# Optimization experiments

Measured on AMD Instinct MI355X. Metric: run time of the kernel, lower is better.

## Reference

```python
import jax, jax.numpy as jnp
import numpy as np

N = 100000   # nodes
D = 128      # in_feats
H = 128      # hidden_size
E = 500000   # message edges
EP = 100000  # positive pair edges
EN = 500000  # negative pair edges


def setup_inputs() -> dict:
    key = jax.random.key(0)
    ks = jax.random.split(key, 20)
    s = 1.0 / np.sqrt(H)
    f32 = jnp.float32
    inp = {
        "x": jax.random.normal(ks[0], (N, D), f32),
        "src": jax.random.randint(ks[1], (E,), 0, N, jnp.int32),
        "dst": jax.random.randint(ks[2], (E,), 0, N, jnp.int32),
        "pos_src": jax.random.randint(ks[3], (EP,), 0, N, jnp.int32),
        "pos_dst": jax.random.randint(ks[4], (EP,), 0, N, jnp.int32),
        "neg_src": jax.random.randint(ks[5], (EN,), 0, N, jnp.int32),
        "neg_dst": jax.random.randint(ks[6], (EN,), 0, N, jnp.int32),
        # SAGEConv layer 0 (in->hid) and layer 1 (hid->hid)
        "W_self0": jax.random.normal(ks[7], (D, H), f32) * s,
        "W_neigh0": jax.random.normal(ks[8], (D, H), f32) * s,
        "b0": jnp.zeros((H,), f32),
        "W_self1": jax.random.normal(ks[9], (H, H), f32) * s,
        "W_neigh1": jax.random.normal(ks[10], (H, H), f32) * s,
        "b1": jnp.zeros((H,), f32),
        # EdgeDecoder MLP: hid->hid->hid->1
        "dW1": jax.random.normal(ks[11], (H, H), f32) * s,
        "db1": jnp.zeros((H,), f32),
        "dW2": jax.random.normal(ks[12], (H, H), f32) * s,
        "db2": jnp.zeros((H,), f32),
        "dW3": jax.random.normal(ks[13], (H, 1), f32) * s,
        "db3": jnp.zeros((1,), f32),
    }
    return inp


def _sage_mean(h, src, dst, W_self, W_neigh, b, n_nodes):
    # mean-aggregate neighbor features: gather src feats, segment-sum over dst
    agg = jax.ops.segment_sum(h[src], dst, num_segments=n_nodes)       # [N, d]
    deg = jax.ops.segment_sum(jnp.ones((src.shape[0],), h.dtype), dst,
                              num_segments=n_nodes)                     # [N]
    h_neigh = agg / jnp.maximum(deg, 1.0)[:, None]
    return h @ W_self + h_neigh @ W_neigh + b


def _edge_decode(h, e_src, e_dst, W1, b1, W2, b2, W3, b3):
    z = h[e_src] * h[e_dst]                    # [E_pair, H]
    z = jax.nn.relu(z @ W1 + b1)
    z = jax.nn.relu(z @ W2 + b2)
    return z @ W3 + b3                         # [E_pair, 1]


def reference(x, src, dst, pos_src, pos_dst, neg_src, neg_dst,
              W_self0, W_neigh0, b0, W_self1, W_neigh1, b1,
              dW1, db1, dW2, db2, dW3, db3):
    n = x.shape[0]
    h = jax.nn.relu(_sage_mean(x, src, dst, W_self0, W_neigh0, b0, n))
    h = _sage_mean(h, src, dst, W_self1, W_neigh1, b1, n)  # no act on last layer
    h_pos = _edge_decode(h, pos_src, pos_dst, dW1, db1, dW2, db2, dW3, db3)
    h_neg = _edge_decode(h, neg_src, neg_dst, dW1, db1, dW2, db2, dW3, db3)
    return (h_pos, h_neg)
```

## Files before the change

### kernel.cpp

```cpp
#include <hip/hip_runtime.h>
#include <hip/hip_bf16.h>

#define HD 128

typedef unsigned int u32;
typedef unsigned short u16;
typedef __attribute__((ext_vector_type(8))) short short8;
typedef __attribute__((ext_vector_type(4))) float f32x4;

__device__ __forceinline__ float bf2f(u16 u) {
    return __uint_as_float(((u32)u) << 16);
}
__device__ __forceinline__ u16 f2bf(float f) {
    u32 u = __float_as_uint(f);
    u32 r = (u + 0x7fffu + ((u >> 16) & 1u)) >> 16;
    return (u16)r;
}
__device__ __forceinline__ u32 pk2bf(float lo, float hi) {
    __hip_bfloat162 h = __float22bfloat162_rn(make_float2(lo, hi));
    union { __hip_bfloat162 h; u32 u; } cv; cv.h = h;
    return cv.u;
}
__device__ __forceinline__ u32 hmul2(u32 a, u32 b) {
    union { u32 u; __hip_bfloat162 h; } x, y, r;
    x.u = a; y.u = b;
    r.h = __hmul2(x.h, y.h);
    return r.u;
}
__device__ __forceinline__ float ldf(const void* p, size_t i, bool f32m) {
    return f32m ? ((const float*)p)[i] : bf2f(((const u16*)p)[i]);
}
__device__ __forceinline__ int swz(int row, int col) {
    return row * 128 + ((((col >> 3) ^ (row & 7)) << 3) | (col & 7));
}
__device__ __forceinline__ void acc8_bf16(uint4 v, float* a) {
    a[0] += __uint_as_float(v.x << 16); a[1] += __uint_as_float(v.x & 0xffff0000u);
    a[2] += __uint_as_float(v.y << 16); a[3] += __uint_as_float(v.y & 0xffff0000u);
    a[4] += __uint_as_float(v.z << 16); a[5] += __uint_as_float(v.z & 0xffff0000u);
    a[6] += __uint_as_float(v.w << 16); a[7] += __uint_as_float(v.w & 0xffff0000u);
}

__global__ void detect_mode(const u32* __restrict__ x, int* __restrict__ mode) {
    __shared__ int cnt_s;
    if (threadIdx.x == 0) cnt_s = 0;
    __syncthreads();
    u32 e = (x[threadIdx.x] >> 23) & 0xFFu;
    if (e >= 90u && e < 170u) atomicAdd(&cnt_s, 1);
    __syncthreads();
    if (threadIdx.x == 0) mode[0] = (cnt_s >= 128) ? 1 : 0;
}

__global__ void pack_w6(const void* __restrict__ W0, const void* __restrict__ W1,
                        const void* __restrict__ W2, const void* __restrict__ W3,
                        const void* __restrict__ W4, const void* __restrict__ W5,
                        u16* __restrict__ out, const int* __restrict__ gmode) {
    const bool f32m = gmode[0] != 0;
    int gid = blockIdx.x * 256 + threadIdx.x;
    if (gid >= 6 * 16384) return;
    int sel = gid >> 14, idx = gid & 16383;
    const void* W = sel == 0 ? W0 : sel == 1 ? W1 : sel == 2 ? W2 :
                    sel == 3 ? W3 : sel == 4 ? W4 : W5;
    int j = idx & 7, lane = (idx >> 3) & 63, ks = (idx >> 9) & 3, nt = idx >> 11;
    int k = ks * 32 + (lane >> 4) * 8 + j;
    int n = nt * 16 + (lane & 15);
    out[gid] = f2bf(ldf(W, (size_t)k * HD + n, f32m));
}

__global__ void cnt_count(const int* __restrict__ dst, int* __restrict__ cnt, int e) {
    int i = blockIdx.x * 256 + threadIdx.x;
    if (i < e) atomicAdd(&cnt[dst[i]], 1);
}

__global__ void scan_blocks(const int* __restrict__ cnt, int* __restrict__ rowptr,
                            int* __restrict__ bsum, int n) {
    __shared__ int s[256];
    int t = threadIdx.x, gid = blockIdx.x * 256 + t;
    int v = (gid < n) ? cnt[gid] : 0;
    s[t] = v; __syncthreads();
    #pragma unroll
    for (int off = 1; off < 256; off <<= 1) {
        int x = (t >= off) ? s[t - off] : 0;
        __syncthreads();
        s[t] += x;
        __syncthreads();
    }
    if (gid < n) rowptr[gid] = s[t] - v;
    if (t == 255) bsum[blockIdx.x] = s[255];
}

__global__ void scan_bsum(int* __restrict__ bsum, int nb) {
    __shared__ int s[1024];
    __shared__ int carry;
    int t = threadIdx.x;
    if (t == 0) carry = 0;
    __syncthreads();
    for (int base = 0; base < nb; base += 1024) {
        int i = base + t;
        int v = (i < nb) ? bsum[i] : 0;
        s[t] = v; __syncthreads();
        #pragma unroll
        for (int off = 1; off < 1024; off <<= 1) {
            int x = (t >= off) ? s[t - off] : 0;
            __syncthreads();
            s[t] += x;
            __syncthreads();
        }
        if (i < nb) bsum[i] = carry + s[t] - v;
        __syncthreads();
        if (t == 0) carry += s[1023];
        __syncthreads();
    }
}

__global__ void scan_add(int* __restrict__ rowptr, const int* __restrict__ bsum,
                         int* __restrict__ cur, int n, int e) {
    int gid = blockIdx.x * 256 + threadIdx.x;
    if (gid < n) {
        int v = rowptr[gid] + bsum[blockIdx.x];
        rowptr[gid] = v;
        cur[gid] = v;
    } else if (gid == n) {
        rowptr[n] = e;
    }
}

__global__ void csr_fill(const int* __restrict__ src, const int* __restrict__ dst,
                         int* __restrict__ cur, int* __restrict__ cidx, int e) {
    int i = blockIdx.x * 256 + threadIdx.x;
    if (i >= e) return;
    int p = atomicAdd(&cur[dst[i]], 1);
    cidx[p] = src[i];
}

template <bool RELU>
__global__ __launch_bounds__(256) void sage_mfma(
    const void* __restrict__ X, const int* __restrict__ rowptr,
    const int* __restrict__ cidx,
    const u16* __restrict__ Wsp, const u16* __restrict__ Wnp,
    const void* __restrict__ bias, u16* __restrict__ hout,
    const int* __restrict__ gmode, int use_mode, int n) {
    __shared__ u16 z[64 * 128];
    const bool f32m = gmode[0] != 0;
    const bool inf32 = use_mode && f32m;
    const int t = threadIdx.x;
    const int n0 = blockIdx.x * 64;
    const int lane = t & 63;
    const int w = t >> 6;
    const int cl = lane & 15, quad = lane >> 4;
    const int l16 = lane & 15, g = lane >> 4;

    #pragma unroll
    for (int i = 0; i < 4; i++) {
        int idx = t + i * 256;
        int e = idx >> 4, sg = (idx & 15) * 8;
        int node = n0 + e;
        uint4 p = make_uint4(0, 0, 0, 0);
        if (node < n) {
            if (inf32) {
                const float* xp = (const float*)X + (size_t)node * HD + sg;
                float4 v0 = *(const float4*)xp, v1 = *(const float4*)(xp + 4);
                p.x = pk2bf(v0.x, v0.y); p.y = pk2bf(v0.z, v0.w);
                p.z = pk2bf(v1.x, v1.y); p.w = pk2bf(v1.z, v1.w);
            } else {
                p = *(const uint4*)((const u16*)X + (size_t)node * HD + sg);
            }
        }
        *(uint4*)&z[swz(e, sg)] = p;
    }
    __syncthreads();

    f32x4 acc[2][4];
    #pragma unroll
    for (int ft = 0; ft < 2; ft++) {
        int f0 = w * 32 + ft * 16 + quad * 4;
        f32x4 bv;
        bv[0] = ldf(bias, f0 + 0, f32m);
        bv[1] = ldf(bias, f0 + 1, f32m);
        bv[2] = ldf(bias, f0 + 2, f32m);
        bv[3] = ldf(bias, f0 + 3, f32m);
        #pragma unroll
        for (int et = 0; et < 4; et++) acc[ft][et] = bv;
    }
    #pragma unroll
    for (int ks = 0; ks < 4; ks++) {
        short8 a[2], b[4];
        #pragma unroll
        for (int ft = 0; ft < 2; ft++)
            a[ft] = ((const short8*)Wsp)[((w * 2 + ft) * 4 + ks) * 64 + lane];
        #pragma unroll
        for (int et = 0; et < 4; et++)
            b[et] = *(const short8*)&z[swz(et * 16 + cl, ks * 32 + quad * 8)];
        #pragma unroll
        for (int ft = 0; ft < 2; ft++)
            #pragma unroll
            for (int et = 0; et < 4; et++)
                acc[ft][et] = __builtin_amdgcn_mfma_f32_16x16x32_bf16(
                    a[ft], b[et], acc[ft][et], 0, 0, 0);
    }
    __syncthreads();

    #pragma unroll 1
    for (int r = 0; r < 4; r++) {
        int e = w * 16 + r * 4 + g;
        int node = n0 + e;
        float a[8] = {0.f, 0.f, 0.f, 0.f, 0.f, 0.f, 0.f, 0.f};
        int deg = 0;
        if (node < n) {
            int s0 = rowptr[node], s1 = rowptr[node + 1];
            deg = s1 - s0;
            int i = s0;
            if (inf32) {
                for (; i + 1 < s1; i += 2) {
                    const float* pA = (const float*)X + (size_t)cidx[i] * HD + l16 * 8;
                    const float* pB = (const float*)X + (size_t)cidx[i + 1] * HD + l16 * 8;
                    float4 a0 = *(const float4*)pA, a1 = *(const float4*)(pA + 4);
                    float4 b0 = *(const float4*)pB, b1 = *(const float4*)(pB + 4);
                    a[0] += a0.x + b0.x; a[1] += a0.y + b0.y;
                    a[2] += a0.z + b0.z; a[3] += a0.w + b0.w;
                    a[4] += a1.x + b1.x; a[5] += a1.y + b1.y;
                    a[6] += a1.z + b1.z; a[7] += a1.w + b1.w;
                }
                if (i < s1) {
                    const float* pA = (const float*)X + (size_t)cidx[i] * HD + l16 * 8;
                    float4 a0 = *(const float4*)pA, a1 = *(const float4*)(pA + 4);
                    a[0] += a0.x; a[1] += a0.y; a[2] += a0.z; a[3] += a0.w;
                    a[4] += a1.x; a[5] += a1.y; a[6] += a1.z; a[7] += a1.w;
                }
            } else {
                for (; i + 1 < s1; i += 2) {
                    uint4 vA = *(const uint4*)((const u16*)X + (size_t)cidx[i] * HD + l16 * 8);
                    uint4 vB = *(const uint4*)((const u16*)X + (size_t)cidx[i + 1] * HD + l16 * 8);
                    acc8_bf16(vA, a);
                    acc8_bf16(vB, a);
                }
                if (i < s1) {
                    uint4 vA = *(const uint4*)((const u16*)X + (size_t)cidx[i] * HD + l16 * 8);
                    acc8_bf16(vA, a);
                }
            }
        }
        float iv = 1.f / fmaxf((float)deg, 1.f);
        uint4 o;
        o.x = pk2bf(a[0] * iv, a[1] * iv);
        o.y = pk2bf(a[2] * iv, a[3] * iv);
        o.z = pk2bf(a[4] * iv, a[5] * iv);
        o.w = pk2bf(a[6] * iv, a[7] * iv);
        *(uint4*)&z[swz(e, l16 * 8)] = o;
    }
    __syncthreads();

    #pragma unroll
    for (int ks = 0; ks < 4; ks++) {
        short8 a[2], b[4];
        #pragma unroll
        for (int ft = 0; ft < 2; ft++)
            a[ft] = ((const short8*)Wnp)[((w * 2 + ft) * 4 + ks) * 64 + lane];
        #pragma unroll
        for (int et = 0; et < 4; et++)
            b[et] = *(const short8*)&z[swz(et * 16 + cl, ks * 32 + quad * 8)];
        #pragma unroll
        for (int ft = 0; ft < 2; ft++)
            #pragma unroll
            for (int et = 0; et < 4; et++)
                acc[ft][et] = __builtin_amdgcn_mfma_f32_16x16x32_bf16(
                    a[ft], b[et], acc[ft][et], 0, 0, 0);
    }
    __syncthreads();

    #pragma unroll
    for (int ft = 0; ft < 2; ft++) {
        int f0 = w * 32 + ft * 16 + quad * 4;
        #pragma unroll
        for (int et = 0; et < 4; et++) {
            f32x4 v = acc[ft][et];
            float v0 = RELU ? fmaxf(v[0], 0.f) : v[0];
            float v1 = RELU ? fmaxf(v[1], 0.f) : v[1];
            float v2 = RELU ? fmaxf(v[2], 0.f) : v[2];
            float v3 = RELU ? fmaxf(v[3], 0.f) : v[3];
            *(uint2*)&z[swz(et * 16 + cl, f0)] =
                make_uint2(pk2bf(v0, v1), pk2bf(v2, v3));
        }
    }
    __syncthreads();
    #pragma unroll
    for (int i = 0; i < 4; i++) {
        int idx = t + i * 256;
        int e = idx >> 4, sg = (idx & 15) * 8;
        int node = n0 + e;
        if (node < n)
            *(uint4*)&hout[(size_t)node * HD + sg] = *(const uint4*)&z[swz(e, sg)];
    }
}

__global__ __launch_bounds__(256) void edge_decode_mfma(
    const u16* __restrict__ h,
    const int* __restrict__ psrc, const int* __restrict__ pdst, int ep, int PB,
    const int* __restrict__ nsrc, const int* __restrict__ ndst, int en,
    const u16* __restrict__ W1p, const void* __restrict__ b1,
    const u16* __restrict__ W2p, const void* __restrict__ b2,
    const void* __restrict__ W3, const void* __restrict__ b3,
    void* __restrict__ out, const int* __restrict__ gmode) {
    __shared__ u16 zA[64 * 128];
    __shared__ float psum[256];
    const bool f32m = gmode[0] != 0;
    const int t = threadIdx.x;
    const int b = blockIdx.x;
    const int* esrc; const int* edst; int e0, obase, ne;
    if (b < PB) { esrc = psrc; edst = pdst; e0 = b * 64;        obase = 0;  ne = ep; }
    else        { esrc = nsrc; edst = ndst; e0 = (b - PB) * 64; obase = ep; ne = en; }
    const int lane = t & 63;
    const int w = t >> 6;
    const int cl = lane & 15, quad = lane >> 4;

    #pragma unroll
    for (int i = 0; i < 4; i++) {
        int idx = t + i * 256;
        int e = idx >> 4, sg = (idx & 15) * 8;
        int eg = e0 + e;
        uint4 z = make_uint4(0, 0, 0, 0);
        if (eg < ne) {
            int s = esrc[eg], d = edst[eg];
            uint4 a  = *(const uint4*)(h + (size_t)s * HD + sg);
            uint4 bv = *(const uint4*)(h + (size_t)d * HD + sg);
            z.x = hmul2(a.x, bv.x); z.y = hmul2(a.y, bv.y);
            z.z = hmul2(a.z, bv.z); z.w = hmul2(a.w, bv.w);
        }
        *(uint4*)&zA[swz(e, sg)] = z;
    }
    __syncthreads();

    f32x4 acc[2][4];
    #pragma unroll
    for (int ft = 0; ft < 2; ft++) {
        int f0 = w * 32 + ft * 16 + quad * 4;
        f32x4 bv;
        bv[0] = ldf(b1, f0 + 0, f32m);
        bv[1] = ldf(b1, f0 + 1, f32m);
        bv[2] = ldf(b1, f0 + 2, f32m);
        bv[3] = ldf(b1, f0 + 3, f32m);
        #pragma unroll
        for (int et = 0; et < 4; et++) acc[ft][et] = bv;
    }
    #pragma unroll
    for (int ks = 0; ks < 4; ks++) {
        short8 a[2], bb[4];
        #pragma unroll
        for (int ft = 0; ft < 2; ft++)
            a[ft] = ((const short8*)W1p)[((w * 2 + ft) * 4 + ks) * 64 + lane];
        #pragma unroll
        for (int et = 0; et < 4; et++)
            bb[et] = *(const short8*)&zA[swz(et * 16 + cl, ks * 32 + quad * 8)];
        #pragma unroll
        for (int ft = 0; ft < 2; ft++)
            #pragma unroll
            for (int et = 0; et < 4; et++)
                acc[ft][et] = __builtin_amdgcn_mfma_f32_16x16x32_bf16(
                    a[ft], bb[et], acc[ft][et], 0, 0, 0);
    }
    __syncthreads();

    #pragma unroll
    for (int ft = 0; ft < 2; ft++) {
        int f0 = w * 32 + ft * 16 + quad * 4;
        #pragma unroll
        for (int et = 0; et < 4; et++) {
            f32x4 v = acc[ft][et];
            *(uint2*)&zA[swz(et * 16 + cl, f0)] = make_uint2(
                pk2bf(fmaxf(v[0], 0.f), fmaxf(v[1], 0.f)),
                pk2bf(fmaxf(v[2], 0.f), fmaxf(v[3], 0.f)));
        }
    }
    __syncthreads();

    #pragma unroll
    for (int ft = 0; ft < 2; ft++) {
        int f0 = w * 32 + ft * 16 + quad * 4;
        f32x4 bv;
        bv[0] = ldf(b2, f0 + 0, f32m);
        bv[1] = ldf(b2, f0 + 1, f32m);
        bv[2] = ldf(b2, f0 + 2, f32m);
        bv[3] = ldf(b2, f0 + 3, f32m);
        #pragma unroll
        for (int et = 0; et < 4; et++) acc[ft][et] = bv;
    }
    #pragma unroll
    for (int ks = 0; ks < 4; ks++) {
        short8 a[2], bb[4];
        #pragma unroll
        for (int ft = 0; ft < 2; ft++)
            a[ft] = ((const short8*)W2p)[((w * 2 + ft) * 4 + ks) * 64 + lane];
        #pragma unroll
        for (int et = 0; et < 4; et++)
            bb[et] = *(const short8*)&zA[swz(et * 16 + cl, ks * 32 + quad * 8)];
        #pragma unroll
        for (int ft = 0; ft < 2; ft++)
            #pragma unroll
            for (int et = 0; et < 4; et++)
                acc[ft][et] = __builtin_amdgcn_mfma_f32_16x16x32_bf16(
                    a[ft], bb[et], acc[ft][et], 0, 0, 0);
    }
    float p[4] = {0.f, 0.f, 0.f, 0.f};
    #pragma unroll
    for (int ft = 0; ft < 2; ft++) {
        int f0 = w * 32 + ft * 16 + quad * 4;
        float w3v0 = ldf(W3, f0 + 0, f32m);
        float w3v1 = ldf(W3, f0 + 1, f32m);
        float w3v2 = ldf(W3, f0 + 2, f32m);
        float w3v3 = ldf(W3, f0 + 3, f32m);
        #pragma unroll
        for (int et = 0; et < 4; et++) {
            f32x4 v = acc[ft][et];
            p[et] = fmaf(fmaxf(v[0], 0.f), w3v0, p[et]);
            p[et] = fmaf(fmaxf(v[1], 0.f), w3v1, p[et]);
            p[et] = fmaf(fmaxf(v[2], 0.f), w3v2, p[et]);
            p[et] = fmaf(fmaxf(v[3], 0.f), w3v3, p[et]);
        }
    }
    #pragma unroll
    for (int et = 0; et < 4; et++) {
        p[et] += __shfl_xor(p[et], 16);
        p[et] += __shfl_xor(p[et], 32);
    }
    if (lane < 16) {
        #pragma unroll
        for (int et = 0; et < 4; et++)
            psum[w * 64 + et * 16 + lane] = p[et];
    }
    __syncthreads();
    if (t < 64) {
        int eg = e0 + t;
        if (eg < ne) {
            float sum = ldf(b3, 0, f32m) + (psum[t] + psum[64 + t])
                      + (psum[128 + t] + psum[192 + t]);
            if (f32m) ((float*)out)[obase + eg] = sum;
            else      ((u16*)out)[obase + eg]   = f2bf(sum);
        }
    }
}

extern "C" void kernel_launch(void* const* d_in, const int* in_sizes, int n_in,
                              void* d_out, int out_size, void* d_ws, size_t ws_size,
                              hipStream_t stream) {
    const void* x      = d_in[0];
    const int* src     = (const int*)d_in[1];
    const int* dst     = (const int*)d_in[2];
    const int* pos_src = (const int*)d_in[3];
    const int* pos_dst = (const int*)d_in[4];
    const int* neg_src = (const int*)d_in[5];
    const int* neg_dst = (const int*)d_in[6];
    const void* Ws0 = d_in[7];
    const void* Wn0 = d_in[8];
    const void* b0  = d_in[9];
    const void* Ws1 = d_in[10];
    const void* Wn1 = d_in[11];
    const void* b1  = d_in[12];
    const void* dW1 = d_in[13];
    const void* db1 = d_in[14];
    const void* dW2 = d_in[15];
    const void* db2 = d_in[16];
    const void* dW3 = d_in[17];
    const void* db3 = d_in[18];

    const int n  = in_sizes[0] / HD;
    const int e  = in_sizes[1];
    const int ep = in_sizes[3];
    const int en = in_sizes[5];
    const int NB = (n + 255) / 256;
    const int PB = (ep + 63) / 64, NDB = (en + 63) / 64;

    char* base = (char*)d_ws;
    u16* h2 = (u16*)d_ws;
    u16* h1 = h2 + (size_t)n * HD;
    size_t off = (size_t)n * HD * 4;
    int* mode = (int*)(base + off);      off += 16;
    int* rowptr = (int*)(base + off);    off += (size_t)(n + 1) * 4; off = (off + 15) & ~(size_t)15;
    int* cur = (int*)(base + off);       off += (size_t)n * 4;       off = (off + 15) & ~(size_t)15;
    int* cidx = (int*)(base + off);      off += (size_t)e * 4;       off = (off + 15) & ~(size_t)15;
    int* bsum = (int*)(base + off);      off += (size_t)NB * 4;      off = (off + 15) & ~(size_t)15;
    u16* Wpk  = (u16*)(base + off);
    u16* W1p  = Wpk;
    u16* W2p  = Wpk + 16384;
    u16* Ws0p = Wpk + 2 * 16384;
    u16* Wn0p = Wpk + 3 * 16384;
    u16* Ws1p = Wpk + 4 * 16384;
    u16* Wn1p = Wpk + 5 * 16384;

    detect_mode<<<dim3(1), dim3(256), 0, stream>>>((const u32*)x, mode);

    hipMemsetAsync(cur, 0, (size_t)n * 4, stream);
    cnt_count<<<dim3((e + 255) / 256), dim3(256), 0, stream>>>(dst, cur, e);
    scan_blocks<<<dim3(NB), dim3(256), 0, stream>>>(cur, rowptr, bsum, n);
    scan_bsum<<<dim3(1), dim3(1024), 0, stream>>>(bsum, NB);
    scan_add<<<dim3((n + 256) / 256), dim3(256), 0, stream>>>(rowptr, bsum, cur, n, e);
    csr_fill<<<dim3((e + 255) / 256), dim3(256), 0, stream>>>(src, dst, cur, cidx, e);

    pack_w6<<<dim3(384), dim3(256), 0, stream>>>(dW1, dW2, Ws0, Wn0, Ws1, Wn1, Wpk, mode);

    sage_mfma<true><<<dim3((n + 63) / 64), dim3(256), 0, stream>>>(
        x, rowptr, cidx, Ws0p, Wn0p, b0, h1, mode, 1, n);

    sage_mfma<false><<<dim3((n + 63) / 64), dim3(256), 0, stream>>>(
        h1, rowptr, cidx, Ws1p, Wn1p, b1, h2, mode, 0, n);

    edge_decode_mfma<<<dim3(PB + NDB), dim3(256), 0, stream>>>(
        h2, pos_src, pos_dst, ep, PB, neg_src, neg_dst, en,
        W1p, db1, W2p, db2, dW3, db3, d_out, mode);
}
```

Before: 349.6 us.

## Pre-cast input to bf16, stage CSR indices in LDS, interleave two-node gathers

Adds a cast_x kernel that converts the fp32 input features to bf16 once, so the first SAGE layer's neighbour gathers read half as many bytes as the fp32 rows they read before. Inside sage_mfma, each block stages its rowptr slice and up to 896 column indices in shared memory, with a fallback to global memory past that cap. The aggregation loop now processes two destination nodes at once, giving more independent gather loads in flight. The cost is an extra full pass over x and workspace reuse of the h2 buffer as the bf16 copy of x.

```diff
diff --git a/kernel.cpp b/kernel.cpp
--- a/kernel.cpp
+++ b/kernel.cpp
@@ -2,6 +2,7 @@
 #include <hip/hip_bf16.h>
 
 #define HD 128
+#define CIDX_CAP 896
 
 typedef unsigned int u32;
 typedef unsigned short u16;
@@ -39,6 +40,14 @@
     a[4] += __uint_as_float(v.z << 16); a[5] += __uint_as_float(v.z & 0xffff0000u);
     a[6] += __uint_as_float(v.w << 16); a[7] += __uint_as_float(v.w & 0xffff0000u);
 }
+__device__ __forceinline__ uint4 ldrow16(const u16* __restrict__ Xb, int node, int colo) {
+    return *(const uint4*)(Xb + (size_t)node * HD + colo);
+}
+__device__ __forceinline__ int gc(const int* __restrict__ cidx,
+                                  const int* cx_s, int cbase, int j) {
+    int o = j - cbase;
+    return (o < CIDX_CAP) ? cx_s[o] : cidx[j];
+}
 
 __global__ void detect_mode(const u32* __restrict__ x, int* __restrict__ mode) {
     __shared__ int cnt_s;
@@ -48,6 +57,21 @@
     if (e >= 90u && e < 170u) atomicAdd(&cnt_s, 1);
     __syncthreads();
     if (threadIdx.x == 0) mode[0] = (cnt_s >= 128) ? 1 : 0;
+}
+
+__global__ void cast_x(const float* __restrict__ x, u16* __restrict__ xb,
+                       const int* __restrict__ gmode, int total8) {
+    if (gmode[0] == 0) return;
+    int i = blockIdx.x * 256 + threadIdx.x;
+    int stride = gridDim.x * 256;
+    for (; i < total8; i += stride) {
+        const float* p = x + (size_t)i * 8;
+        float4 v0 = *(const float4*)p, v1 = *(const float4*)(p + 4);
+        uint4 o;
+        o.x = pk2bf(v0.x, v0.y); o.y = pk2bf(v0.z, v0.w);
+        o.z = pk2bf(v1.x, v1.y); o.w = pk2bf(v1.z, v1.w);
+        *(uint4*)(xb + (size_t)i * 8) = o;
+    }
 }
 
 __global__ void pack_w6(const void* __restrict__ W0, const void* __restrict__ W1,
@@ -134,14 +158,16 @@
 
 template <bool RELU>
 __global__ __launch_bounds__(256) void sage_mfma(
-    const void* __restrict__ X, const int* __restrict__ rowptr,
-    const int* __restrict__ cidx,
+    const void* __restrict__ X, const u16* __restrict__ Xc,
+    const int* __restrict__ rowptr, const int* __restrict__ cidx,
     const u16* __restrict__ Wsp, const u16* __restrict__ Wnp,
     const void* __restrict__ bias, u16* __restrict__ hout,
-    const int* __restrict__ gmode, int use_mode, int n) {
+    const int* __restrict__ gmode, int n) {
     __shared__ u16 z[64 * 128];
+    __shared__ int rp_s[65];
+    __shared__ int cx_s[CIDX_CAP];
     const bool f32m = gmode[0] != 0;
-    const bool inf32 = use_mode && f32m;
+    const u16* Xb = f32m ? Xc : (const u16*)X;
     const int t = threadIdx.x;
     const int n0 = blockIdx.x * 64;
     const int lane = t & 63;
@@ -149,25 +175,29 @@
     const int cl = lane & 15, quad = lane >> 4;
     const int l16 = lane & 15, g = lane >> 4;
 
+    if (t < 65) {
+        int idx = n0 + t;
+        rp_s[t] = rowptr[idx < n ? idx : n];
+    }
+
     #pragma unroll
     for (int i = 0; i < 4; i++) {
         int idx = t + i * 256;
         int e = idx >> 4, sg = (idx & 15) * 8;
         int node = n0 + e;
         uint4 p = make_uint4(0, 0, 0, 0);
-        if (node < n) {
-            if (inf32) {
-                const float* xp = (const float*)X + (size_t)node * HD + sg;
-                float4 v0 = *(const float4*)xp, v1 = *(const float4*)(xp + 4);
-                p.x = pk2bf(v0.x, v0.y); p.y = pk2bf(v0.z, v0.w);
-                p.z = pk2bf(v1.x, v1.y); p.w = pk2bf(v1.z, v1.w);
-            } else {
-                p = *(const uint4*)((const u16*)X + (size_t)node * HD + sg);
-            }
-        }
+        if (node < n)
+            p = *(const uint4*)(Xb + (size_t)node * HD + sg);
         *(uint4*)&z[swz(e, sg)] = p;
     }
     __syncthreads();
+
+    const int cbase = rp_s[0];
+    {
+        int ccnt = rp_s[64] - cbase;
+        if (ccnt > CIDX_CAP) ccnt = CIDX_CAP;
+        for (int j = t; j < ccnt; j += 256) cx_s[j] = cidx[cbase + j];
+    }
 
     f32x4 acc[2][4];
     #pragma unroll
@@ -200,52 +230,65 @@
     __syncthreads();
 
     #pragma unroll 1
-    for (int r = 0; r < 4; r++) {
-        int e = w * 16 + r * 4 + g;
-        int node = n0 + e;
-        float a[8] = {0.f, 0.f, 0.f, 0.f, 0.f, 0.f, 0.f, 0.f};
-        int deg = 0;
-        if (node < n) {
-            int s0 = rowptr[node], s1 = rowptr[node + 1];
-            deg = s1 - s0;
-            int i = s0;
-            if (inf32) {
-                for (; i + 1 < s1; i += 2) {
-                    const float* pA = (const float*)X + (size_t)cidx[i] * HD + l16 * 8;
-                    const float* pB = (const float*)X + (size_t)cidx[i + 1] * HD + l16 * 8;
-                    float4 a0 = *(const float4*)pA, a1 = *(const float4*)(pA + 4);
-                    float4 b0 = *(const float4*)pB, b1 = *(const float4*)(pB + 4);
-                    a[0] += a0.x + b0.x; a[1] += a0.y + b0.y;
-                    a[2] += a0.z + b0.z; a[3] += a0.w + b0.w;
-                    a[4] += a1.x + b1.x; a[5] += a1.y + b1.y;
-                    a[6] += a1.z + b1.z; a[7] += a1.w + b1.w;
-                }
-                if (i < s1) {
-                    const float* pA = (const float*)X + (size_t)cidx[i] * HD + l16 * 8;
-                    float4 a0 = *(const float4*)pA, a1 = *(const float4*)(pA + 4);
-                    a[0] += a0.x; a[1] += a0.y; a[2] += a0.z; a[3] += a0.w;
-                    a[4] += a1.x; a[5] += a1.y; a[6] += a1.z; a[7] += a1.w;
-                }
-            } else {
-                for (; i + 1 < s1; i += 2) {
-                    uint4 vA = *(const uint4*)((const u16*)X + (size_t)cidx[i] * HD + l16 * 8);
-                    uint4 vB = *(const uint4*)((const u16*)X + (size_t)cidx[i + 1] * HD + l16 * 8);
-                    acc8_bf16(vA, a);
-                    acc8_bf16(vB, a);
-                }
-                if (i < s1) {
-                    uint4 vA = *(const uint4*)((const u16*)X + (size_t)cidx[i] * HD + l16 * 8);
-                    acc8_bf16(vA, a);
-                }
-            }
-        }
-        float iv = 1.f / fmaxf((float)deg, 1.f);
-        uint4 o;
-        o.x = pk2bf(a[0] * iv, a[1] * iv);
-        o.y = pk2bf(a[2] * iv, a[3] * iv);
-        o.z = pk2bf(a[4] * iv, a[5] * iv);
-        o.w = pk2bf(a[6] * iv, a[7] * iv);
-        *(uint4*)&z[swz(e, l16 * 8)] = o;
+    for (int r2 = 0; r2 < 2; r2++) {
+        int eA = w * 16 + r2 * 8 + g;
+        int eB = eA + 4;
+        int sA0 = rp_s[eA], sA1 = rp_s[eA + 1];
+        int sB0 = rp_s[eB], sB1 = rp_s[eB + 1];
+        float aA[8] = {0.f, 0.f, 0.f, 0.f, 0.f, 0.f, 0.f, 0.f};
+        float aB[8] = {0.f, 0.f, 0.f, 0.f, 0.f, 0.f, 0.f, 0.f};
+        int iA = sA0, iB = sB0;
+        const int colo = l16 * 8;
+        while (iA + 1 < sA1 && iB + 1 < sB1) {
+            int c0 = gc(cidx, cx_s, cbase, iA);
+            int c1 = gc(cidx, cx_s, cbase, iA + 1);
+            int c2 = gc(cidx, cx_s, cbase, iB);
+            int c3 = gc(cidx, cx_s, cbase, iB + 1);
+            uint4 v0 = ldrow16(Xb, c0, colo);
+            uint4 v1 = ldrow16(Xb, c1, colo);
+            uint4 v2 = ldrow16(Xb, c2, colo);
+            uint4 v3 = ldrow16(Xb, c3, colo);
+            acc8_bf16(v0, aA); acc8_bf16(v1, aA);
+            acc8_bf16(v2, aB); acc8_bf16(v3, aB);
+            iA += 2; iB += 2;
+        }
+        for (; iA + 1 < sA1; iA += 2) {
+            int c0 = gc(cidx, cx_s, cbase, iA);
+            int c1 = gc(cidx, cx_s, cbase, iA + 1);
+            uint4 v0 = ldrow16(Xb, c0, colo);
+            uint4 v1 = ldrow16(Xb, c1, colo);
+            acc8_bf16(v0, aA); acc8_bf16(v1, aA);
+        }
+        if (iA < sA1) {
+            int c0 = gc(cidx, cx_s, cbase, iA);
+            uint4 v0 = ldrow16(Xb, c0, colo);
+            acc8_bf16(v0, aA);
+        }
+        for (; iB + 1 < sB1; iB += 2) {
+            int c0 = gc(cidx, cx_s, cbase, iB);
+            int c1 = gc(cidx, cx_s, cbase, iB + 1);
+            uint4 v0 = ldrow16(Xb, c0, colo);
+            uint4 v1 = ldrow16(Xb, c1, colo);
+            acc8_bf16(v0, aB); acc8_bf16(v1, aB);
+        }
+        if (iB < sB1) {
+            int c0 = gc(cidx, cx_s, cbase, iB);
+            uint4 v0 = ldrow16(Xb, c0, colo);
+            acc8_bf16(v0, aB);
+        }
+        float ivA = 1.f / fmaxf((float)(sA1 - sA0), 1.f);
+        float ivB = 1.f / fmaxf((float)(sB1 - sB0), 1.f);
+        uint4 oA, oB;
+        oA.x = pk2bf(aA[0] * ivA, aA[1] * ivA);
+        oA.y = pk2bf(aA[2] * ivA, aA[3] * ivA);
+        oA.z = pk2bf(aA[4] * ivA, aA[5] * ivA);
+        oA.w = pk2bf(aA[6] * ivA, aA[7] * ivA);
+        oB.x = pk2bf(aB[0] * ivB, aB[1] * ivB);
+        oB.y = pk2bf(aB[2] * ivB, aB[3] * ivB);
+        oB.z = pk2bf(aB[4] * ivB, aB[5] * ivB);
+        oB.w = pk2bf(aB[6] * ivB, aB[7] * ivB);
+        *(uint4*)&z[swz(eA, colo)] = oA;
+        *(uint4*)&z[swz(eB, colo)] = oB;
     }
     __syncthreads();
 
@@ -471,6 +514,7 @@
     char* base = (char*)d_ws;
     u16* h2 = (u16*)d_ws;
     u16* h1 = h2 + (size_t)n * HD;
+    u16* xb = h2;
     size_t off = (size_t)n * HD * 4;
     int* mode = (int*)(base + off);      off += 16;
     int* rowptr = (int*)(base + off);    off += (size_t)(n + 1) * 4; off = (off + 15) & ~(size_t)15;
@@ -496,11 +540,14 @@
 
     pack_w6<<<dim3(384), dim3(256), 0, stream>>>(dW1, dW2, Ws0, Wn0, Ws1, Wn1, Wpk, mode);
 
+    cast_x<<<dim3(2048), dim3(256), 0, stream>>>(
+        (const float*)x, xb, mode, n * (HD / 8));
+
     sage_mfma<true><<<dim3((n + 63) / 64), dim3(256), 0, stream>>>(
-        x, rowptr, cidx, Ws0p, Wn0p, b0, h1, mode, 1, n);
+        x, xb, rowptr, cidx, Ws0p, Wn0p, b0, h1, mode, n);
 
     sage_mfma<false><<<dim3((n + 63) / 64), dim3(256), 0, stream>>>(
-        h1, rowptr, cidx, Ws1p, Wn1p, b1, h2, mode, 0, n);
+        h1, h1, rowptr, cidx, Ws1p, Wn1p, b1, h2, mode, n);
 
     edge_decode_mfma<<<dim3(PB + NDB), dim3(256), 0, stream>>>(
         h2, pos_src, pos_dst, ep, PB, neg_src, neg_dst, en,
```

Result: no change. 350.9 us (+0.4%).

## Split SAGE layers into separate gather-mean and GEMM kernels with bf16 input cast

Applied to the files above, without the earlier changes.

Moves the neighbor mean aggregation out of the fused SAGE MFMA kernel into a standalone agg_mean kernel with 16 rows per block and 4-way unrolled gathers. The layer-0 input is first cast to bf16 once, so gathers read half-size rows instead of fp32 ones. The GEMM kernel then reads both the self and mean tiles from global memory. This aims to raise occupancy and gather parallelism, decoupled from the MFMA tile, at the cost of extra kernel launches and an intermediate mean buffer written and read per layer. sage_gemm writes its output in place into its own input buffer; this looks safe because each block reads only its own 64 rows before overwriting them.

```diff
diff --git a/kernel.cpp b/kernel.cpp
--- a/kernel.cpp
+++ b/kernel.cpp
@@ -48,6 +48,28 @@
     if (e >= 90u && e < 170u) atomicAdd(&cnt_s, 1);
     __syncthreads();
     if (threadIdx.x == 0) mode[0] = (cnt_s >= 128) ? 1 : 0;
+}
+
+__global__ void cast_x(const void* __restrict__ x, u16* __restrict__ xb,
+                       const int* __restrict__ gmode, int total8) {
+    const bool f32m = gmode[0] != 0;
+    int i = blockIdx.x * 256 + threadIdx.x;
+    int stride = gridDim.x * 256;
+    if (f32m) {
+        for (; i < total8; i += stride) {
+            const float* p = (const float*)x + (size_t)i * 8;
+            float4 v0 = *(const float4*)p, v1 = *(const float4*)(p + 4);
+            uint4 o;
+            o.x = pk2bf(v0.x, v0.y); o.y = pk2bf(v0.z, v0.w);
+            o.z = pk2bf(v1.x, v1.y); o.w = pk2bf(v1.z, v1.w);
+            *(uint4*)(xb + (size_t)i * 8) = o;
+        }
+    } else {
+        for (; i < total8; i += stride) {
+            *(uint4*)(xb + (size_t)i * 8) =
+                *(const uint4*)((const u16*)x + (size_t)i * 8);
+        }
+    }
 }
 
 __global__ void pack_w6(const void* __restrict__ W0, const void* __restrict__ W1,
@@ -132,40 +154,72 @@
     cidx[p] = src[i];
 }
 
+__global__ __launch_bounds__(256, 8) void agg_mean(
+    const u16* __restrict__ X, const int* __restrict__ rowptr,
+    const int* __restrict__ cidx, u16* __restrict__ M, int n) {
+    const int t = threadIdx.x;
+    const int row = blockIdx.x * 16 + (t >> 4);
+    if (row >= n) return;
+    const int colo = (t & 15) * 8;
+    const int s0 = rowptr[row], s1 = rowptr[row + 1];
+    float a[8] = {0.f, 0.f, 0.f, 0.f, 0.f, 0.f, 0.f, 0.f};
+    int i = s0;
+    for (; i + 3 < s1; i += 4) {
+        int c0 = cidx[i], c1 = cidx[i + 1], c2 = cidx[i + 2], c3 = cidx[i + 3];
+        uint4 v0 = *(const uint4*)(X + (size_t)c0 * HD + colo);
+        uint4 v1 = *(const uint4*)(X + (size_t)c1 * HD + colo);
+        uint4 v2 = *(const uint4*)(X + (size_t)c2 * HD + colo);
+        uint4 v3 = *(const uint4*)(X + (size_t)c3 * HD + colo);
+        acc8_bf16(v0, a); acc8_bf16(v1, a);
+        acc8_bf16(v2, a); acc8_bf16(v3, a);
+    }
+    if (i + 1 < s1) {
+        int c0 = cidx[i], c1 = cidx[i + 1];
+        uint4 v0 = *(const uint4*)(X + (size_t)c0 * HD + colo);
+        uint4 v1 = *(const uint4*)(X + (size_t)c1 * HD + colo);
+        acc8_bf16(v0, a); acc8_bf16(v1, a);
+        i += 2;
+    }
+    if (i < s1) {
+        uint4 v0 = *(const uint4*)(X + (size_t)cidx[i] * HD + colo);
+        acc8_bf16(v0, a);
+    }
+    float iv = 1.f / fmaxf((float)(s1 - s0), 1.f);
+    uint4 o;
+    o.x = pk2bf(a[0] * iv, a[1] * iv);
+    o.y = pk2bf(a[2] * iv, a[3] * iv);
+    o.z = pk2bf(a[4] * iv, a[5] * iv);
+    o.w = pk2bf(a[6] * iv, a[7] * iv);
+    *(uint4*)(M + (size_t)row * HD + colo) = o;
+}
+
 template <bool RELU>
-__global__ __launch_bounds__(256) void sage_mfma(
-    const void* __restrict__ X, const int* __restrict__ rowptr,
-    const int* __restrict__ cidx,
+__global__ __launch_bounds__(256, 4) void sage_gemm(
+    const u16* __restrict__ X, const u16* __restrict__ M,
     const u16* __restrict__ Wsp, const u16* __restrict__ Wnp,
     const void* __restrict__ bias, u16* __restrict__ hout,
-    const int* __restrict__ gmode, int use_mode, int n) {
-    __shared__ u16 z[64 * 128];
+    const int* __restrict__ gmode, int n) {
+    __shared__ u16 zx[64 * 128];
+    __shared__ u16 zm[64 * 128];
     const bool f32m = gmode[0] != 0;
-    const bool inf32 = use_mode && f32m;
     const int t = threadIdx.x;
     const int n0 = blockIdx.x * 64;
     const int lane = t & 63;
     const int w = t >> 6;
     const int cl = lane & 15, quad = lane >> 4;
-    const int l16 = lane & 15, g = lane >> 4;
 
     #pragma unroll
     for (int i = 0; i < 4; i++) {
         int idx = t + i * 256;
         int e = idx >> 4, sg = (idx & 15) * 8;
         int node = n0 + e;
-        uint4 p = make_uint4(0, 0, 0, 0);
+        uint4 px = make_uint4(0, 0, 0, 0), pm = make_uint4(0, 0, 0, 0);
         if (node < n) {
-            if (inf32) {
-                const float* xp = (const float*)X + (size_t)node * HD + sg;
-                float4 v0 = *(const float4*)xp, v1 = *(const float4*)(xp + 4);
-                p.x = pk2bf(v0.x, v0.y); p.y = pk2bf(v0.z, v0.w);
-                p.z = pk2bf(v1.x, v1.y); p.w = pk2bf(v1.z, v1.w);
-            } else {
-                p = *(const uint4*)((const u16*)X + (size_t)node * HD + sg);
-            }
-        }
-        *(uint4*)&z[swz(e, sg)] = p;
+            px = *(const uint4*)(X + (size_t)node * HD + sg);
+            pm = *(const uint4*)(M + (size_t)node * HD + sg);
+        }
+        *(uint4*)&zx[swz(e, sg)] = px;
+        *(uint4*)&zm[swz(e, sg)] = pm;
     }
     __syncthreads();
 
@@ -189,7 +243,7 @@
             a[ft] = ((const short8*)Wsp)[((w * 2 + ft) * 4 + ks) * 64 + lane];
         #pragma unroll
         for (int et = 0; et < 4; et++)
-            b[et] = *(const short8*)&z[swz(et * 16 + cl, ks * 32 + quad * 8)];
+            b[et] = *(const short8*)&zx[swz(et * 16 + cl, ks * 32 + quad * 8)];
         #pragma unroll
         for (int ft = 0; ft < 2; ft++)
             #pragma unroll
@@ -197,58 +251,6 @@
                 acc[ft][et] = __builtin_amdgcn_mfma_f32_16x16x32_bf16(
                     a[ft], b[et], acc[ft][et], 0, 0, 0);
     }
-    __syncthreads();
-
-    #pragma unroll 1
-    for (int r = 0; r < 4; r++) {
-        int e = w * 16 + r * 4 + g;
-        int node = n0 + e;
-        float a[8] = {0.f, 0.f, 0.f, 0.f, 0.f, 0.f, 0.f, 0.f};
-        int deg = 0;
-        if (node < n) {
-            int s0 = rowptr[node], s1 = rowptr[node + 1];
-            deg = s1 - s0;
-            int i = s0;
-            if (inf32) {
-                for (; i + 1 < s1; i += 2) {
-                    const float* pA = (const float*)X + (size_t)cidx[i] * HD + l16 * 8;
-                    const float* pB = (const float*)X + (size_t)cidx[i + 1] * HD + l16 * 8;
-                    float4 a0 = *(const float4*)pA, a1 = *(const float4*)(pA + 4);
-                    float4 b0 = *(const float4*)pB, b1 = *(const float4*)(pB + 4);
-                    a[0] += a0.x + b0.x; a[1] += a0.y + b0.y;
-                    a[2] += a0.z + b0.z; a[3] += a0.w + b0.w;
-                    a[4] += a1.x + b1.x; a[5] += a1.y + b1.y;
-                    a[6] += a1.z + b1.z; a[7] += a1.w + b1.w;
-                }
-                if (i < s1) {
-                    const float* pA = (const float*)X + (size_t)cidx[i] * HD + l16 * 8;
-                    float4 a0 = *(const float4*)pA, a1 = *(const float4*)(pA + 4);
-                    a[0] += a0.x; a[1] += a0.y; a[2] += a0.z; a[3] += a0.w;
-                    a[4] += a1.x; a[5] += a1.y; a[6] += a1.z; a[7] += a1.w;
-                }
-            } else {
-                for (; i + 1 < s1; i += 2) {
-                    uint4 vA = *(const uint4*)((const u16*)X + (size_t)cidx[i] * HD + l16 * 8);
-                    uint4 vB = *(const uint4*)((const u16*)X + (size_t)cidx[i + 1] * HD + l16 * 8);
-                    acc8_bf16(vA, a);
-                    acc8_bf16(vB, a);
-                }
-                if (i < s1) {
-                    uint4 vA = *(const uint4*)((const u16*)X + (size_t)cidx[i] * HD + l16 * 8);
-                    acc8_bf16(vA, a);
-                }
-            }
-        }
-        float iv = 1.f / fmaxf((float)deg, 1.f);
-        uint4 o;
-        o.x = pk2bf(a[0] * iv, a[1] * iv);
-        o.y = pk2bf(a[2] * iv, a[3] * iv);
-        o.z = pk2bf(a[4] * iv, a[5] * iv);
-        o.w = pk2bf(a[6] * iv, a[7] * iv);
-        *(uint4*)&z[swz(e, l16 * 8)] = o;
-    }
-    __syncthreads();
-
     #pragma unroll
     for (int ks = 0; ks < 4; ks++) {
         short8 a[2], b[4];
@@ -257,7 +259,7 @@
             a[ft] = ((const short8*)Wnp)[((w * 2 + ft) * 4 + ks) * 64 + lane];
         #pragma unroll
         for (int et = 0; et < 4; et++)
-            b[et] = *(const short8*)&z[swz(et * 16 + cl, ks * 32 + quad * 8)];
+            b[et] = *(const short8*)&zm[swz(et * 16 + cl, ks * 32 + quad * 8)];
         #pragma unroll
         for (int ft = 0; ft < 2; ft++)
             #pragma unroll
@@ -277,7 +279,7 @@
             float v1 = RELU ? fmaxf(v[1], 0.f) : v[1];
             float v2 = RELU ? fmaxf(v[2], 0.f) : v[2];
             float v3 = RELU ? fmaxf(v[3], 0.f) : v[3];
-            *(uint2*)&z[swz(et * 16 + cl, f0)] =
+            *(uint2*)&zx[swz(et * 16 + cl, f0)] =
                 make_uint2(pk2bf(v0, v1), pk2bf(v2, v3));
         }
     }
@@ -288,7 +290,7 @@
         int e = idx >> 4, sg = (idx & 15) * 8;
         int node = n0 + e;
         if (node < n)
-            *(uint4*)&hout[(size_t)node * HD + sg] = *(const uint4*)&z[swz(e, sg)];
+            *(uint4*)&hout[(size_t)node * HD + sg] = *(const uint4*)&zx[swz(e, sg)];
     }
 }
 
@@ -469,8 +471,8 @@
     const int PB = (ep + 63) / 64, NDB = (en + 63) / 64;
 
     char* base = (char*)d_ws;
-    u16* h2 = (u16*)d_ws;
-    u16* h1 = h2 + (size_t)n * HD;
+    u16* R1 = (u16*)d_ws;
+    u16* R2 = R1 + (size_t)n * HD;
     size_t off = (size_t)n * HD * 4;
     int* mode = (int*)(base + off);      off += 16;
     int* rowptr = (int*)(base + off);    off += (size_t)(n + 1) * 4; off = (off + 15) & ~(size_t)15;
@@ -496,13 +498,17 @@
 
     pack_w6<<<dim3(384), dim3(256), 0, stream>>>(dW1, dW2, Ws0, Wn0, Ws1, Wn1, Wpk, mode);
 
-    sage_mfma<true><<<dim3((n + 63) / 64), dim3(256), 0, stream>>>(
-        x, rowptr, cidx, Ws0p, Wn0p, b0, h1, mode, 1, n);
-
-    sage_mfma<false><<<dim3((n + 63) / 64), dim3(256), 0, stream>>>(
-        h1, rowptr, cidx, Ws1p, Wn1p, b1, h2, mode, 0, n);
+    cast_x<<<dim3(2048), dim3(256), 0, stream>>>(x, R1, mode, n * (HD / 8));
+
+    agg_mean<<<dim3((n + 15) / 16), dim3(256), 0, stream>>>(R1, rowptr, cidx, R2, n);
+    sage_gemm<true><<<dim3((n + 63) / 64), dim3(256), 0, stream>>>(
+        R1, R2, Ws0p, Wn0p, b0, R1, mode, n);
+
+    agg_mean<<<dim3((n + 15) / 16), dim3(256), 0, stream>>>(R1, rowptr, cidx, R2, n);
+    sage_gemm<false><<<dim3((n + 63) / 64), dim3(256), 0, stream>>>(
+        R1, R2, Ws1p, Wn1p, b1, R1, mode, n);
 
     edge_decode_mfma<<<dim3(PB + NDB), dim3(256), 0, stream>>>(
-        h2, pos_src, pos_dst, ep, PB, neg_src, neg_dst, en,
+        R1, pos_src, pos_dst, ep, PB, neg_src, neg_dst, en,
         W1p, db1, W2p, db2, dW3, db3, d_out, mode);
 }
```

Measured after the change: 345.0 us, median of 2. No clear change (-1.3%).
